# Performance work log

Measured on AMD Instinct MI355X. Metric: run time of the kernel, lower is better.

Reference implementation:

```python
import jax, jax.numpy as jnp
import numpy as np

N_NODES = 50000
N_EDGES = 1600000
N_GRAPHS = 1000
F_IN = 92      # atom_input_features
WIDTH = 128    # config.width
F_OUT = 64     # output_features
LENGTHSCALE = 8.0  # config.edge_lengthscale


def setup_inputs() -> dict:
    key = jax.random.key(0)
    ks = jax.random.split(key, 12)
    inp = {
        "atom_features": jax.random.normal(ks[0], (N_NODES, F_IN), dtype=jnp.float32),
        "bondlength": jax.random.normal(ks[1], (N_EDGES, 3), dtype=jnp.float32) * 2.0,
        "src": jax.random.randint(ks[2], (N_EDGES,), 0, N_NODES, dtype=jnp.int32),
        "dst": jax.random.randint(ks[3], (N_EDGES,), 0, N_NODES, dtype=jnp.int32),
        "graph_ids": jnp.sort(jax.random.randint(ks[4], (N_NODES,), 0, N_GRAPHS, dtype=jnp.int32)),
        # atom_embedding Linear(F_IN, WIDTH)
        "W0": jax.random.normal(ks[5], (F_IN, WIDTH), dtype=jnp.float32) * 0.05,
        "b0": jnp.zeros((WIDTH,), dtype=jnp.float32),
        # GraphConv layer1 (WIDTH -> WIDTH)
        "W1": jax.random.normal(ks[6], (WIDTH, WIDTH), dtype=jnp.float32) * 0.05,
        "b1": jnp.zeros((WIDTH,), dtype=jnp.float32),
        # GraphConv layer2 (WIDTH -> F_OUT)
        "W2": jax.random.normal(ks[7], (WIDTH, F_OUT), dtype=jnp.float32) * 0.05,
        "b2": jnp.zeros((F_OUT,), dtype=jnp.float32),
    }
    return inp


def _degrees(src, dst, n_nodes):
    ones = jnp.ones(src.shape[0], dtype=jnp.float32)
    out_deg = jax.ops.segment_sum(ones, src, num_segments=n_nodes)
    in_deg = jax.ops.segment_sum(ones, dst, num_segments=n_nodes)
    # DGL GraphConv clamps degrees to min 1 (norm='both')
    return jnp.clip(out_deg, 1.0, None), jnp.clip(in_deg, 1.0, None)


def reference(atom_features, bondlength, src, dst, graph_ids, W0, b0, W1, b1, W2, b2):
    # edge weights: exp(-|r|^2 / lengthscale^2)
    r2 = jnp.sum(bondlength * bondlength, axis=1)  # [E]
    ew = jnp.exp(-r2 / (LENGTHSCALE ** 2))         # [E]

    out_deg, in_deg = _degrees(src, dst, N_NODES)
    norm_src = out_deg ** -0.5  # [N]
    norm_dst = in_deg ** -0.5   # [N]

    # atom embedding
    h = atom_features @ W0 + b0  # [N, WIDTH]

    # GraphConv layer1 (in==out: aggregate then weight), norm='both'
    hs = h * norm_src[:, None]
    m = hs[src] * ew[:, None]                                   # [E, WIDTH]
    agg = jax.ops.segment_sum(m, dst, num_segments=N_NODES)
    x = agg * norm_dst[:, None]
    x = jax.nn.relu(x @ W1 + b1)

    # GraphConv layer2 (in > out: weight first, then aggregate)
    hs = (x * norm_src[:, None]) @ W2                           # [N, F_OUT]
    m = hs[src] * ew[:, None]                                   # [E, F_OUT]
    agg = jax.ops.segment_sum(m, dst, num_segments=N_NODES)
    x = agg * norm_dst[:, None] + b2

    # AvgPooling readout per graph
    cnt = jnp.clip(jax.ops.segment_sum(jnp.ones(N_NODES, jnp.float32), graph_ids, num_segments=N_GRAPHS), 1.0, None)
    pooled = jax.ops.segment_sum(x, graph_ids, num_segments=N_GRAPHS) / cnt[:, None]
    return jnp.squeeze(pooled)  # [N_GRAPHS, F_OUT]
```

## Files before the change

### kernel.cpp

```cpp
#include <hip/hip_runtime.h>
#include <hip/hip_fp16.h>

#define N_NODES  50000
#define N_EDGES  1600000
#define N_GRAPHS 1000
#define F_IN     92
#define WIDTH    128
#define F_OUT    64
#define NBLK_SCAN 196
#define CHUNK    16384
#define NBLK_E   98
#define HPB      25024
#define HWRD     6256
#define BPITCH   50048
#define XPITCH   48

static const size_t ROWP  = 50000;
static const size_t SVAL  = 100004;
static const size_t NSRC  = 150004;
static const size_t NDST  = 200004;
static const size_t BSUM  = 250004;
static const size_t RNK8  = 250260;
static const size_t HD    = 650260;
static const size_t HSR   = 1263348;
static const size_t BASEP = 1876436;
static const size_t CSR   = 3102612;
static const size_t XB    = 6302612;
static const size_t W01   = 8702612;
static const size_t BW1   = 8714388;
static const size_t GAGG  = 8714516;
static const size_t HS2   = 13514516;
static const size_t AGG2  = GAGG;
static const size_t W01P  = 15114516;
static const size_t W2P   = 15120660;

typedef __attribute__((ext_vector_type(8))) _Float16 half8v;
typedef __attribute__((ext_vector_type(4))) float f32x4;

__device__ inline unsigned short f2bf(float f) {
    unsigned u = __float_as_uint(f);
    return (unsigned short)((u + 0x7fff + ((u >> 16) & 1)) >> 16);
}
__device__ inline float bflo(unsigned u) { return __uint_as_float(u << 16); }
__device__ inline float bfhi(unsigned u) { return __uint_as_float(u & 0xffff0000u); }
__device__ inline unsigned short f2h(float f) {
    return __half_as_ushort(__float2half(f));
}
__device__ inline float csr_w(unsigned v) {
    return __half2float(__ushort_as_half((unsigned short)(v >> 16)));
}

__global__ __launch_bounds__(256) void k_hist(const int* __restrict__ src,
                                              const int* __restrict__ dst,
                                              unsigned char* __restrict__ h_dst,
                                              unsigned char* __restrict__ h_src,
                                              unsigned char* __restrict__ rank8) {
    __shared__ unsigned sh[HWRD];
    const bool is_dst = blockIdx.x < NBLK_E;
    const int b = is_dst ? blockIdx.x : blockIdx.x - NBLK_E;
    const int e0 = b * CHUNK;
    const int ecnt = min(CHUNK, N_EDGES - e0);
    for (int i = threadIdx.x; i < HWRD; i += 256) sh[i] = 0;
    __syncthreads();
    const int* __restrict__ idx = is_dst ? dst : src;
    for (int i = threadIdx.x; i < ecnt; i += 256) {
        int v = idx[e0 + i];
        unsigned sh_amt = (v & 7) * 4;
        unsigned old = atomicAdd(&sh[v >> 3], 1u << sh_amt);
        if (is_dst) rank8[e0 + i] = (unsigned char)((old >> sh_amt) & 0xfu);
    }
    __syncthreads();
    unsigned* out = (unsigned*)((is_dst ? h_dst : h_src) + (size_t)b * HPB);
    for (int i = threadIdx.x; i < HWRD; i += 256) out[i] = sh[i];
}

__global__ void k_packX(const float* __restrict__ af, unsigned* __restrict__ xb) {
    int idx = blockIdx.x * blockDim.x + threadIdx.x;
    if (idx >= N_NODES * XPITCH) return;
    int n = idx / XPITCH, c = idx - n * XPITCH;
    unsigned v = 0;
    if (c < 46) {
        const float* p = af + (size_t)n * F_IN + 2 * c;
        v = (unsigned)f2bf(p[0]) | ((unsigned)f2bf(p[1]) << 16);
    }
    xb[idx] = v;
}

__global__ __launch_bounds__(256) void k_reduceScan(const unsigned char* __restrict__ h_dst,
                                                    const unsigned char* __restrict__ h_src,
                                                    unsigned char* __restrict__ basep,
                                                    int* __restrict__ rowp,
                                                    int* __restrict__ bsum,
                                                    float* __restrict__ nsrc,
                                                    float* __restrict__ ndst) {
    __shared__ int sd[256];
    const int t = threadIdx.x;
    const int n = blockIdx.x * 256 + t;
    const bool valid = n < N_NODES;
    unsigned run = 0;
    if (valid) {
        const int byte = n >> 1;
        const int shn = (n & 1) * 4;
        for (int b = 0; b < NBLK_E; ++b) {
            unsigned v = (h_dst[(size_t)b * HPB + byte] >> shn) & 0xfu;
            basep[(size_t)b * BPITCH + n] = (unsigned char)run;
            run += v;
        }
        ndst[n] = rsqrtf((float)max(run, 1u));
        unsigned so = 0;
        for (int b = 0; b < NBLK_E; ++b)
            so += (h_src[(size_t)b * HPB + byte] >> shn) & 0xfu;
        nsrc[n] = rsqrtf((float)max(so, 1u));
    }
    int v = valid ? (int)run : 0;
    sd[t] = v;
    __syncthreads();
    for (int off = 1; off < 256; off <<= 1) {
        int add = (t >= off) ? sd[t - off] : 0;
        __syncthreads();
        sd[t] += add;
        __syncthreads();
    }
    if (valid) rowp[n] = sd[t] - v;
    if (t == 255) bsum[blockIdx.x] = sd[255];
}

__global__ __launch_bounds__(256) void k_scanB(int* __restrict__ bsum) {
    __shared__ int sd[256];
    const int t = threadIdx.x;
    int v = (t < NBLK_SCAN) ? bsum[t] : 0;
    sd[t] = v;
    __syncthreads();
    for (int off = 1; off < 256; off <<= 1) {
        int add = (t >= off) ? sd[t - off] : 0;
        __syncthreads();
        sd[t] += add;
        __syncthreads();
    }
    if (t < NBLK_SCAN) bsum[t] = sd[t] - v;
}

__global__ void k_scanC(int* __restrict__ rowp, const int* __restrict__ bsum) {
    int i = blockIdx.x * blockDim.x + threadIdx.x;
    if (i >= N_NODES) return;
    rowp[i] = rowp[i] + bsum[i >> 8];
    if (i == 0) rowp[N_NODES] = N_EDGES;
}

__global__ void k_fill(const float* __restrict__ bl,
                       const int* __restrict__ src, const int* __restrict__ dst,
                       const unsigned char* __restrict__ rank8,
                       const unsigned char* __restrict__ basep,
                       const int* __restrict__ rowp,
                       const float* __restrict__ nsrc,
                       unsigned* __restrict__ csr) {
    int e = blockIdx.x * blockDim.x + threadIdx.x;
    if (e >= N_EDGES) return;
    float x = bl[3 * e + 0], y = bl[3 * e + 1], z = bl[3 * e + 2];
    int s = src[e], d = dst[e];
    float w = expf(-(x * x + y * y + z * z) * (1.0f / 64.0f)) * nsrc[s];
    int b = e >> 14;
    int p = rowp[d] + (int)basep[(size_t)b * BPITCH + d] + (int)rank8[e];
    csr[p] = (unsigned)s | ((unsigned)f2h(w) << 16);
}

__global__ __launch_bounds__(128) void k_w01(const float* __restrict__ W0,
                                             const float* __restrict__ W1,
                                             const float* __restrict__ b0,
                                             float* __restrict__ w01,
                                             float* __restrict__ bw1) {
    const int t = threadIdx.x;
    const int k = blockIdx.x;
    float acc = 0.0f;
    if (k < F_IN) {
        for (int j = 0; j < WIDTH; ++j)
            acc = fmaf(W0[k * WIDTH + j], W1[j * WIDTH + t], acc);
        w01[k * WIDTH + t] = acc;
    } else {
        for (int j = 0; j < WIDTH; ++j)
            acc = fmaf(b0[j], W1[j * WIDTH + t], acc);
        bw1[t] = acc;
    }
}

__global__ __launch_bounds__(256) void k_prepW(const float* __restrict__ w01,
                                               const float* __restrict__ W2,
                                               unsigned* __restrict__ w01p,
                                               unsigned* __restrict__ w2p) {
    int idx = blockIdx.x * 256 + threadIdx.x;
    if (idx < 6144) {
        int q = idx & 3, lane = (idx >> 2) & 63;
        int rest = idx >> 8;
        int kb = rest % 3, t = rest / 3;
        int k = kb * 32 + ((lane >> 4) * 8) + 2 * q;
        int n = t * 16 + (lane & 15);
        float lo = (k < F_IN) ? w01[k * WIDTH + n] : 0.f;
        float hi = (k + 1 < F_IN) ? w01[(k + 1) * WIDTH + n] : 0.f;
        w01p[idx] = (unsigned)f2h(lo) | ((unsigned)f2h(hi) << 16);
    } else if (idx < 10240) {
        int i2 = idx - 6144;
        int q = i2 & 3, lane = (i2 >> 2) & 63;
        int rest = i2 >> 8;
        int kb = rest & 3, t = rest >> 2;
        int k = kb * 32 + ((lane >> 4) * 8) + 2 * q;
        int n = t * 16 + (lane & 15);
        float lo = W2[k * F_OUT + n];
        float hi = W2[(k + 1) * F_OUT + n];
        w2p[i2] = (unsigned)f2h(lo) | ((unsigned)f2h(hi) << 16);
    }
}

__global__ __launch_bounds__(256) void k_gatherG(const int* __restrict__ rowp,
                                                 const unsigned* __restrict__ csr,
                                                 const unsigned* __restrict__ xb,
                                                 float2* __restrict__ gf2,
                                                 float* __restrict__ S) {
    __shared__ unsigned sb[4][64];
    const int wid = threadIdx.x >> 6;
    const int lane = threadIdx.x & 63;
    const int n = blockIdx.x * 4 + wid;
    const int tc = min(lane, XPITCH - 1);
    unsigned* my = sb[wid];
    const int start = rowp[n], end = rowp[n + 1];
    float2 acc = {0.f, 0.f};
    float ssum = 0.f;
    for (int base = start; base < end; base += 64) {
        const int m = min(64, end - base);
        my[lane] = (lane < m) ? csr[base + lane] : 0u;
        const int mr = (m + 3) & ~3;
        for (int j = 0; j < mr; j += 4) {
            unsigned e0 = my[j], e1 = my[j + 1], e2 = my[j + 2], e3 = my[j + 3];
            unsigned a0 = xb[(size_t)(e0 & 0xFFFFu) * XPITCH + tc];
            unsigned a1 = xb[(size_t)(e1 & 0xFFFFu) * XPITCH + tc];
            unsigned a2 = xb[(size_t)(e2 & 0xFFFFu) * XPITCH + tc];
            unsigned a3 = xb[(size_t)(e3 & 0xFFFFu) * XPITCH + tc];
            float w0 = csr_w(e0), w1 = csr_w(e1), w2 = csr_w(e2), w3 = csr_w(e3);
            acc.x = fmaf(bflo(a0), w0, acc.x);
            acc.y = fmaf(bfhi(a0), w0, acc.y);
            acc.x = fmaf(bflo(a1), w1, acc.x);
            acc.y = fmaf(bfhi(a1), w1, acc.y);
            acc.x = fmaf(bflo(a2), w2, acc.x);
            acc.y = fmaf(bfhi(a2), w2, acc.y);
            acc.x = fmaf(bflo(a3), w3, acc.x);
            acc.y = fmaf(bfhi(a3), w3, acc.y);
            ssum += (w0 + w1) + (w2 + w3);
        }
    }
    if (lane < XPITCH) gf2[(size_t)n * XPITCH + lane] = acc;
    else if (lane == 63) S[n] = ssum;
}

__global__ __launch_bounds__(256) void k_layer1(const float* __restrict__ g,
                                                const float* __restrict__ S,
                                                const float* __restrict__ ndst,
                                                const unsigned* __restrict__ w01p,
                                                const unsigned* __restrict__ w2p,
                                                const float* __restrict__ bw1,
                                                const float* __restrict__ b1,
                                                unsigned short* __restrict__ hs2h) {
    __shared__ unsigned short x2[4][16][136];
    __shared__ float svs[4][16];
    const int wid = threadIdx.x >> 6, lane = threadIdx.x & 63;
    const int row0 = blockIdx.x * 64 + wid * 16;
    const int mn = lane & 15;
    const int kq = lane >> 4;
    if (lane < 16) {
        int r = row0 + lane;
        svs[wid][lane] = (r < N_NODES) ? S[r] * ndst[r] : 0.f;
    }
    const float nd = ndst[min(row0 + mn, N_NODES - 1)];
    const float* grow = g + (size_t)(row0 + mn) * 96;
    half8v a1[3];
#pragma unroll
    for (int kb = 0; kb < 3; ++kb) {
        const float4 p0 = *(const float4*)(grow + kb * 32 + kq * 8);
        const float4 p1 = *(const float4*)(grow + kb * 32 + kq * 8 + 4);
        a1[kb][0] = (_Float16)(p0.x * nd); a1[kb][1] = (_Float16)(p0.y * nd);
        a1[kb][2] = (_Float16)(p0.z * nd); a1[kb][3] = (_Float16)(p0.w * nd);
        a1[kb][4] = (_Float16)(p1.x * nd); a1[kb][5] = (_Float16)(p1.y * nd);
        a1[kb][6] = (_Float16)(p1.z * nd); a1[kb][7] = (_Float16)(p1.w * nd);
    }
    for (int t = 0; t < 8; ++t) {
        const float bwv = bw1[t * 16 + mn];
        const float b1v = b1[t * 16 + mn];
        f32x4 acc = {0.f, 0.f, 0.f, 0.f};
        const unsigned* wp = w01p + ((size_t)t * 3 * 64 + lane) * 4;
#pragma unroll
        for (int kb = 0; kb < 3; ++kb) {
            half8v bf = *(const half8v*)(wp + (size_t)kb * 256);
            acc = __builtin_amdgcn_mfma_f32_16x16x32_f16(a1[kb], bf, acc, 0, 0, 0);
        }
#pragma unroll
        for (int r = 0; r < 4; ++r) {
            float v = acc[r] + svs[wid][kq * 4 + r] * bwv + b1v;
            x2[wid][kq * 4 + r][t * 16 + mn] = f2h(fmaxf(v, 0.f));
        }
    }
    half8v a2[4];
#pragma unroll
    for (int kb = 0; kb < 4; ++kb)
        a2[kb] = *(const half8v*)&x2[wid][mn][kb * 32 + kq * 8];
    for (int t2 = 0; t2 < 4; ++t2) {
        f32x4 acc = {0.f, 0.f, 0.f, 0.f};
        const unsigned* wp = w2p + ((size_t)t2 * 4 * 64 + lane) * 4;
#pragma unroll
        for (int kb = 0; kb < 4; ++kb) {
            half8v bf = *(const half8v*)(wp + (size_t)kb * 256);
            acc = __builtin_amdgcn_mfma_f32_16x16x32_f16(a2[kb], bf, acc, 0, 0, 0);
        }
#pragma unroll
        for (int r = 0; r < 4; ++r) {
            int row = row0 + kq * 4 + r;
            if (row < N_NODES)
                hs2h[(size_t)row * 64 + t2 * 16 + mn] = f2bf(acc[r]);
        }
    }
}

__global__ __launch_bounds__(256) void k_gather2(const int* __restrict__ rowp,
                                                 const unsigned* __restrict__ csr,
                                                 const unsigned* __restrict__ hs2u,
                                                 float2* __restrict__ agg2f2) {
    __shared__ unsigned sb[4][64];
    const int wid = threadIdx.x >> 6;
    const int lane = threadIdx.x & 63;
    const int n = blockIdx.x * 4 + wid;
    const int c = lane & 31;
    const int h = lane >> 5;
    unsigned* my = sb[wid];
    const int start = rowp[n], end = rowp[n + 1];
    float2 acc = {0.f, 0.f};
    for (int base = start; base < end; base += 64) {
        const int m = min(64, end - base);
        my[lane] = (lane < m) ? csr[base + lane] : 0u;
        const int mr = (m + 7) & ~7;
        for (int j = 0; j < mr; j += 8) {
#pragma unroll
            for (int k = 0; k < 4; ++k) {
                unsigned sw = my[j + 2 * k + h];
                unsigned a = hs2u[(size_t)(sw & 0xFFFFu) * 32 + c];
                float w = csr_w(sw);
                acc.x = fmaf(bflo(a), w, acc.x);
                acc.y = fmaf(bfhi(a), w, acc.y);
            }
        }
    }
    acc.x += __shfl_xor(acc.x, 32);
    acc.y += __shfl_xor(acc.y, 32);
    if (lane < 32) agg2f2[(size_t)n * 32 + lane] = acc;
}

__global__ __launch_bounds__(64) void k_pool(const float* __restrict__ agg2,
                                             const float* __restrict__ ndst,
                                             const float* __restrict__ b2,
                                             const int* __restrict__ gid,
                                             float* __restrict__ out) {
    const int g = blockIdx.x;
    const int t = threadIdx.x;
    int lo = 0, hi = N_NODES;
    while (lo < hi) { int mid = (lo + hi) >> 1; if (gid[mid] < g) lo = mid + 1; else hi = mid; }
    const int start = lo;
    hi = N_NODES;
    while (lo < hi) { int mid = (lo + hi) >> 1; if (gid[mid] < g + 1) lo = mid + 1; else hi = mid; }
    const int end = lo;
    float sum = 0.0f;
    for (int n = start; n < end; ++n)
        sum = fmaf(agg2[n * F_OUT + t], ndst[n], sum);
    out[g * F_OUT + t] = (end > start) ? (sum / (float)(end - start) + b2[t]) : 0.0f;
}

extern "C" void kernel_launch(void* const* d_in, const int* in_sizes, int n_in,
                              void* d_out, int out_size, void* d_ws, size_t ws_size,
                              hipStream_t stream) {
    const float* af  = (const float*)d_in[0];
    const float* bl  = (const float*)d_in[1];
    const int*   src = (const int*)d_in[2];
    const int*   dst = (const int*)d_in[3];
    const int*   gid = (const int*)d_in[4];
    const float* W0  = (const float*)d_in[5];
    const float* b0  = (const float*)d_in[6];
    const float* W1  = (const float*)d_in[7];
    const float* b1  = (const float*)d_in[8];
    const float* W2  = (const float*)d_in[9];
    const float* b2  = (const float*)d_in[10];
    float* out = (float*)d_out;
    float* ws  = (float*)d_ws;

    int*            rowp   = (int*)(ws + ROWP);
    float*          S      = ws + SVAL;
    float*          nsrc   = ws + NSRC;
    float*          ndst   = ws + NDST;
    int*            bsum   = (int*)(ws + BSUM);
    unsigned char*  rank8  = (unsigned char*)(ws + RNK8);
    unsigned char*  h_dst  = (unsigned char*)(ws + HD);
    unsigned char*  h_src  = (unsigned char*)(ws + HSR);
    unsigned char*  basep  = (unsigned char*)(ws + BASEP);
    unsigned*       csr    = (unsigned*)(ws + CSR);
    unsigned*       xb     = (unsigned*)(ws + XB);
    float*          w01    = ws + W01;
    float*          bw1    = ws + BW1;
    float*          g      = ws + GAGG;
    unsigned*       hs2u   = (unsigned*)(ws + HS2);
    unsigned short* hs2h   = (unsigned short*)(ws + HS2);
    float*          agg2   = ws + AGG2;
    unsigned*       w01p   = (unsigned*)(ws + W01P);
    unsigned*       w2p    = (unsigned*)(ws + W2P);

    const int EB = (N_EDGES + 255) / 256;
    k_hist<<<2 * NBLK_E, 256, 0, stream>>>(src, dst, h_dst, h_src, rank8);
    k_packX<<<(N_NODES * XPITCH) / 256, 256, 0, stream>>>(af, xb);
    k_reduceScan<<<NBLK_SCAN, 256, 0, stream>>>(h_dst, h_src, basep, rowp, bsum, nsrc, ndst);
    k_scanB<<<1, 256, 0, stream>>>(bsum);
    k_scanC<<<NBLK_SCAN, 256, 0, stream>>>(rowp, bsum);
    k_fill<<<EB, 256, 0, stream>>>(bl, src, dst, rank8, basep, rowp, nsrc, csr);
    k_w01<<<F_IN + 1, 128, 0, stream>>>(W0, W1, b0, w01, bw1);
    k_prepW<<<40, 256, 0, stream>>>(w01, W2, w01p, w2p);
    k_gatherG<<<N_NODES / 4, 256, 0, stream>>>(rowp, csr, xb, (float2*)g, S);
    k_layer1<<<(N_NODES + 63) / 64, 256, 0, stream>>>(g, S, ndst, w01p, w2p, bw1, b1, hs2h);
    k_gather2<<<N_NODES / 4, 256, 0, stream>>>(rowp, csr, hs2u, (float2*)agg2);
    k_pool<<<N_GRAPHS, 64, 0, stream>>>(agg2, ndst, b2, gid, out);
}
```

Before: 317.7 us.

## Build CSR via two-level bucket binning instead of per-chunk histogram scatter

Replaces the dst histogram, per-block base-offset tables, three-kernel scan and random scatter with a two-pass bucket sort. Edges are first binned into 196 buckets of 256 destination nodes using shared-memory counters and global cursors. Each bucket is then sorted locally in LDS to write the CSR, row pointers and dst norms. This removes the large basep and rank8 traffic and the fully random 1.6M-element scatter, at the cost of a fixed per-bucket capacity (9216) that silently drops edges if a bucket overflows, and of non-deterministic edge order within a row.

```diff
diff --git a/kernel.cpp b/kernel.cpp
--- a/kernel.cpp
+++ b/kernel.cpp
@@ -7,32 +7,34 @@
 #define F_IN     92
 #define WIDTH    128
 #define F_OUT    64
-#define NBLK_SCAN 196
 #define CHUNK    16384
 #define NBLK_E   98
 #define HPB      25024
 #define HWRD     6256
-#define BPITCH   50048
 #define XPITCH   48
-
-static const size_t ROWP  = 50000;
-static const size_t SVAL  = 100004;
-static const size_t NSRC  = 150004;
-static const size_t NDST  = 200004;
-static const size_t BSUM  = 250004;
-static const size_t RNK8  = 250260;
-static const size_t HD    = 650260;
-static const size_t HSR   = 1263348;
-static const size_t BASEP = 1876436;
-static const size_t CSR   = 3102612;
-static const size_t XB    = 6302612;
-static const size_t W01   = 8702612;
-static const size_t BW1   = 8714388;
-static const size_t GAGG  = 8714516;
-static const size_t HS2   = 13514516;
+#define BKT      196
+#define CAP      9216
+#define BINCHUNK 4096
+#define NBIN     391
+
+static const size_t CURS  = 0;
+static const size_t CSRB  = 256;
+static const size_t NSRC  = 520;
+static const size_t NDST  = 50520;
+static const size_t SVAL  = 100520;
+static const size_t ROWP  = 150520;
+static const size_t HSR   = 200528;
+static const size_t SGW   = 813616;
+static const size_t SGB   = 2619952;
+static const size_t CSR   = 3071536;
+static const size_t XB    = 4671536;
+static const size_t W01   = 7071536;
+static const size_t BW1   = 7083312;
+static const size_t W01P  = 7083440;
+static const size_t W2P   = 7089584;
+static const size_t GAGG  = 7093680;
+static const size_t HS2   = 11893680;
 static const size_t AGG2  = GAGG;
-static const size_t W01P  = 15114516;
-static const size_t W2P   = 15120660;
 
 typedef __attribute__((ext_vector_type(8))) _Float16 half8v;
 typedef __attribute__((ext_vector_type(4))) float f32x4;
@@ -50,28 +52,35 @@
     return __half2float(__ushort_as_half((unsigned short)(v >> 16)));
 }
 
-__global__ __launch_bounds__(256) void k_hist(const int* __restrict__ src,
-                                              const int* __restrict__ dst,
-                                              unsigned char* __restrict__ h_dst,
-                                              unsigned char* __restrict__ h_src,
-                                              unsigned char* __restrict__ rank8) {
+__global__ void k_init(unsigned* __restrict__ cursor) {
+    cursor[threadIdx.x] = (unsigned)threadIdx.x * CAP;
+}
+
+__global__ __launch_bounds__(256) void k_srcHist(const int* __restrict__ src,
+                                                 unsigned char* __restrict__ h_src) {
     __shared__ unsigned sh[HWRD];
-    const bool is_dst = blockIdx.x < NBLK_E;
-    const int b = is_dst ? blockIdx.x : blockIdx.x - NBLK_E;
-    const int e0 = b * CHUNK;
+    const int e0 = blockIdx.x * CHUNK;
     const int ecnt = min(CHUNK, N_EDGES - e0);
     for (int i = threadIdx.x; i < HWRD; i += 256) sh[i] = 0;
     __syncthreads();
-    const int* __restrict__ idx = is_dst ? dst : src;
     for (int i = threadIdx.x; i < ecnt; i += 256) {
-        int v = idx[e0 + i];
-        unsigned sh_amt = (v & 7) * 4;
-        unsigned old = atomicAdd(&sh[v >> 3], 1u << sh_amt);
-        if (is_dst) rank8[e0 + i] = (unsigned char)((old >> sh_amt) & 0xfu);
-    }
-    __syncthreads();
-    unsigned* out = (unsigned*)((is_dst ? h_dst : h_src) + (size_t)b * HPB);
+        int v = src[e0 + i];
+        atomicAdd(&sh[v >> 3], 1u << ((v & 7) * 4));
+    }
+    __syncthreads();
+    unsigned* out = (unsigned*)(h_src + (size_t)blockIdx.x * HPB);
     for (int i = threadIdx.x; i < HWRD; i += 256) out[i] = sh[i];
+}
+
+__global__ __launch_bounds__(256) void k_nsrc(const unsigned char* __restrict__ h_src,
+                                              float* __restrict__ nsrc) {
+    int n = blockIdx.x * 256 + threadIdx.x;
+    if (n >= N_NODES) return;
+    const int byte = n >> 1, shn = (n & 1) * 4;
+    unsigned so = 0;
+    for (int b = 0; b < NBLK_E; ++b)
+        so += (h_src[(size_t)b * HPB + byte] >> shn) & 0xfu;
+    nsrc[n] = rsqrtf((float)max(so, 1u));
 }
 
 __global__ void k_packX(const float* __restrict__ af, unsigned* __restrict__ xb) {
@@ -86,82 +95,111 @@
     xb[idx] = v;
 }
 
-__global__ __launch_bounds__(256) void k_reduceScan(const unsigned char* __restrict__ h_dst,
-                                                    const unsigned char* __restrict__ h_src,
-                                                    unsigned char* __restrict__ basep,
-                                                    int* __restrict__ rowp,
-                                                    int* __restrict__ bsum,
-                                                    float* __restrict__ nsrc,
-                                                    float* __restrict__ ndst) {
+__global__ __launch_bounds__(256) void k_bin(const float* __restrict__ bl,
+                                             const int* __restrict__ src,
+                                             const int* __restrict__ dst,
+                                             const float* __restrict__ nsrc,
+                                             unsigned* __restrict__ cursor,
+                                             unsigned* __restrict__ sgw,
+                                             unsigned char* __restrict__ sgb) {
+    __shared__ unsigned hcnt[256];
+    __shared__ unsigned gbase[256];
+    const int t = threadIdx.x;
+    const int e0 = blockIdx.x * BINCHUNK;
+    hcnt[t] = 0;
+    __syncthreads();
+    unsigned entry[16], meta[16];
+#pragma unroll
+    for (int i = 0; i < 16; ++i) {
+        int e = e0 + t + i * 256;
+        meta[i] = 0xFFFFFFFFu;
+        if (e < N_EDGES) {
+            float x = bl[3 * e], y = bl[3 * e + 1], z = bl[3 * e + 2];
+            int s = src[e], d = dst[e];
+            float w = expf(-(x * x + y * y + z * z) * (1.0f / 64.0f)) * nsrc[s];
+            entry[i] = (unsigned)s | ((unsigned)f2h(w) << 16);
+            int bkt = d >> 8;
+            unsigned r = atomicAdd(&hcnt[bkt], 1u);
+            meta[i] = ((unsigned)bkt << 20) | ((unsigned)(d & 255) << 12) | r;
+        }
+    }
+    __syncthreads();
+    if (t < BKT) gbase[t] = hcnt[t] ? atomicAdd(&cursor[t], hcnt[t]) : 0u;
+    __syncthreads();
+#pragma unroll
+    for (int i = 0; i < 16; ++i) {
+        if (meta[i] != 0xFFFFFFFFu) {
+            unsigned bkt = meta[i] >> 20;
+            unsigned slot = gbase[bkt] + (meta[i] & 0xFFFu);
+            if (slot < (bkt + 1) * CAP) {
+                sgw[slot] = entry[i];
+                sgb[slot] = (unsigned char)((meta[i] >> 12) & 0xFFu);
+            }
+        }
+    }
+}
+
+__global__ __launch_bounds__(256) void k_bscan(const unsigned* __restrict__ cursor,
+                                               int* __restrict__ csrb,
+                                               int* __restrict__ rowp) {
     __shared__ int sd[256];
     const int t = threadIdx.x;
-    const int n = blockIdx.x * 256 + t;
-    const bool valid = n < N_NODES;
-    unsigned run = 0;
-    if (valid) {
-        const int byte = n >> 1;
-        const int shn = (n & 1) * 4;
-        for (int b = 0; b < NBLK_E; ++b) {
-            unsigned v = (h_dst[(size_t)b * HPB + byte] >> shn) & 0xfu;
-            basep[(size_t)b * BPITCH + n] = (unsigned char)run;
-            run += v;
-        }
-        ndst[n] = rsqrtf((float)max(run, 1u));
-        unsigned so = 0;
-        for (int b = 0; b < NBLK_E; ++b)
-            so += (h_src[(size_t)b * HPB + byte] >> shn) & 0xfu;
-        nsrc[n] = rsqrtf((float)max(so, 1u));
-    }
-    int v = valid ? (int)run : 0;
-    sd[t] = v;
+    int c = (t < BKT) ? (int)(cursor[t] - (unsigned)t * CAP) : 0;
+    sd[t] = c;
     __syncthreads();
     for (int off = 1; off < 256; off <<= 1) {
-        int add = (t >= off) ? sd[t - off] : 0;
+        int v = (t >= off) ? sd[t - off] : 0;
         __syncthreads();
-        sd[t] += add;
+        sd[t] += v;
         __syncthreads();
     }
-    if (valid) rowp[n] = sd[t] - v;
-    if (t == 255) bsum[blockIdx.x] = sd[255];
-}
-
-__global__ __launch_bounds__(256) void k_scanB(int* __restrict__ bsum) {
-    __shared__ int sd[256];
-    const int t = threadIdx.x;
-    int v = (t < NBLK_SCAN) ? bsum[t] : 0;
-    sd[t] = v;
+    if (t < BKT) csrb[t] = sd[t] - c;
+    if (t == 0) rowp[N_NODES] = N_EDGES;
+}
+
+__global__ __launch_bounds__(256) void k_csr(const unsigned* __restrict__ cursor,
+                                             const int* __restrict__ csrb,
+                                             const unsigned* __restrict__ sgw,
+                                             const unsigned char* __restrict__ sgb,
+                                             unsigned* __restrict__ csr,
+                                             int* __restrict__ rowp,
+                                             float* __restrict__ ndst) {
+    __shared__ unsigned se[CAP];
+    __shared__ unsigned char sd8[CAP];
+    __shared__ unsigned dh[256];
+    __shared__ unsigned dcur[256];
+    __shared__ int sscan[256];
+    const int b = blockIdx.x, t = threadIdx.x;
+    const int cnt = (int)(cursor[b] - (unsigned)b * CAP);
+    const int base = csrb[b];
+    for (int i = t; i < cnt; i += 256) {
+        se[i] = sgw[(size_t)b * CAP + i];
+        sd8[i] = sgb[(size_t)b * CAP + i];
+    }
+    dh[t] = 0;
+    __syncthreads();
+    for (int i = t; i < cnt; i += 256) atomicAdd(&dh[sd8[i]], 1u);
+    __syncthreads();
+    int v = (int)dh[t];
+    sscan[t] = v;
     __syncthreads();
     for (int off = 1; off < 256; off <<= 1) {
-        int add = (t >= off) ? sd[t - off] : 0;
+        int a = (t >= off) ? sscan[t - off] : 0;
         __syncthreads();
-        sd[t] += add;
+        sscan[t] += a;
         __syncthreads();
     }
-    if (t < NBLK_SCAN) bsum[t] = sd[t] - v;
-}
-
-__global__ void k_scanC(int* __restrict__ rowp, const int* __restrict__ bsum) {
-    int i = blockIdx.x * blockDim.x + threadIdx.x;
-    if (i >= N_NODES) return;
-    rowp[i] = rowp[i] + bsum[i >> 8];
-    if (i == 0) rowp[N_NODES] = N_EDGES;
-}
-
-__global__ void k_fill(const float* __restrict__ bl,
-                       const int* __restrict__ src, const int* __restrict__ dst,
-                       const unsigned char* __restrict__ rank8,
-                       const unsigned char* __restrict__ basep,
-                       const int* __restrict__ rowp,
-                       const float* __restrict__ nsrc,
-                       unsigned* __restrict__ csr) {
-    int e = blockIdx.x * blockDim.x + threadIdx.x;
-    if (e >= N_EDGES) return;
-    float x = bl[3 * e + 0], y = bl[3 * e + 1], z = bl[3 * e + 2];
-    int s = src[e], d = dst[e];
-    float w = expf(-(x * x + y * y + z * z) * (1.0f / 64.0f)) * nsrc[s];
-    int b = e >> 14;
-    int p = rowp[d] + (int)basep[(size_t)b * BPITCH + d] + (int)rank8[e];
-    csr[p] = (unsigned)s | ((unsigned)f2h(w) << 16);
+    dcur[t] = (unsigned)(sscan[t] - v);
+    const int node = b * 256 + t;
+    if (node < N_NODES) {
+        rowp[node] = base + (sscan[t] - v);
+        ndst[node] = rsqrtf((float)max((unsigned)v, 1u));
+    }
+    __syncthreads();
+    for (int i = t; i < cnt; i += 256) {
+        unsigned pos = atomicAdd(&dcur[sd8[i]], 1u);
+        csr[(size_t)base + pos] = se[i];
+    }
 }
 
 __global__ __launch_bounds__(128) void k_w01(const float* __restrict__ W0,
@@ -386,33 +424,33 @@
     float* out = (float*)d_out;
     float* ws  = (float*)d_ws;
 
-    int*            rowp   = (int*)(ws + ROWP);
-    float*          S      = ws + SVAL;
+    unsigned*       cursor = (unsigned*)(ws + CURS);
+    int*            csrb   = (int*)(ws + CSRB);
     float*          nsrc   = ws + NSRC;
     float*          ndst   = ws + NDST;
-    int*            bsum   = (int*)(ws + BSUM);
-    unsigned char*  rank8  = (unsigned char*)(ws + RNK8);
-    unsigned char*  h_dst  = (unsigned char*)(ws + HD);
+    float*          S      = ws + SVAL;
+    int*            rowp   = (int*)(ws + ROWP);
     unsigned char*  h_src  = (unsigned char*)(ws + HSR);
-    unsigned char*  basep  = (unsigned char*)(ws + BASEP);
+    unsigned*       sgw    = (unsigned*)(ws + SGW);
+    unsigned char*  sgb    = (unsigned char*)(ws + SGB);
     unsigned*       csr    = (unsigned*)(ws + CSR);
     unsigned*       xb     = (unsigned*)(ws + XB);
     float*          w01    = ws + W01;
     float*          bw1    = ws + BW1;
+    unsigned*       w01p   = (unsigned*)(ws + W01P);
+    unsigned*       w2p    = (unsigned*)(ws + W2P);
     float*          g      = ws + GAGG;
     unsigned*       hs2u   = (unsigned*)(ws + HS2);
     unsigned short* hs2h   = (unsigned short*)(ws + HS2);
     float*          agg2   = ws + AGG2;
-    unsigned*       w01p   = (unsigned*)(ws + W01P);
-    unsigned*       w2p    = (unsigned*)(ws + W2P);
-
-    const int EB = (N_EDGES + 255) / 256;
-    k_hist<<<2 * NBLK_E, 256, 0, stream>>>(src, dst, h_dst, h_src, rank8);
+
+    k_init<<<1, 256, 0, stream>>>(cursor);
+    k_srcHist<<<NBLK_E, 256, 0, stream>>>(src, h_src);
     k_packX<<<(N_NODES * XPITCH) / 256, 256, 0, stream>>>(af, xb);
-    k_reduceScan<<<NBLK_SCAN, 256, 0, stream>>>(h_dst, h_src, basep, rowp, bsum, nsrc, ndst);
-    k_scanB<<<1, 256, 0, stream>>>(bsum);
-    k_scanC<<<NBLK_SCAN, 256, 0, stream>>>(rowp, bsum);
-    k_fill<<<EB, 256, 0, stream>>>(bl, src, dst, rank8, basep, rowp, nsrc, csr);
+    k_nsrc<<<BKT, 256, 0, stream>>>(h_src, nsrc);
+    k_bin<<<NBIN, 256, 0, stream>>>(bl, src, dst, nsrc, cursor, sgw, sgb);
+    k_bscan<<<1, 256, 0, stream>>>(cursor, csrb, rowp);
+    k_csr<<<BKT, 256, 0, stream>>>(cursor, csrb, sgw, sgb, csr, rowp, ndst);
     k_w01<<<F_IN + 1, 128, 0, stream>>>(W0, W1, b0, w01, bw1);
     k_prepW<<<40, 256, 0, stream>>>(w01, W2, w01p, w2p);
     k_gatherG<<<N_NODES / 4, 256, 0, stream>>>(rowp, csr, xb, (float2*)g, S);
```

New measurement: 291.3 us. 1.09x faster.
